# Kernel optimization log

Measured on AMD Instinct MI355X. Metric: run time of the kernel, lower is better.

## Reference

```python
import jax, jax.numpy as jnp
import numpy as np

V, N, D, K = 4, 2048, 128, 10
NEG = -1e9


def setup_inputs() -> dict:
    key = jax.random.key(0)
    k1, k2, k3, k4, k5 = jax.random.split(key, 5)
    aligned = jax.random.normal(k1, (V, N, D), dtype=jnp.float32)
    C = jax.random.uniform(k2, (V, V, N, N), dtype=jnp.float32)
    s = 1.0 / np.sqrt(D)
    WQ = jax.random.normal(k3, (V, D, D), dtype=jnp.float32) * s
    WK = jax.random.normal(k4, (V, D, D), dtype=jnp.float32) * s
    WV = jax.random.normal(k5, (V, D, D), dtype=jnp.float32) * s
    return {"aligned": aligned, "C": C, "WQ": WQ, "WK": WK, "WV": WV}


def _forward(aligned, C, WQ, WK, WV):
    # per-view linear projections (nn.Linear: x @ W^T), W: (V, out, in)
    Qn = jnp.einsum('vnd,ved->vne', aligned, WQ)  # (V,N,D)
    Kn = jnp.einsum('vnd,ved->vne', aligned, WK)
    Vn = jnp.einsum('vnd,ved->vne', aligned, WV)

    # per-pair row-wise top-k sparsify + row-normalize
    vals, idx = jax.lax.top_k(C, K)  # (V,V,N,K)
    pi = jnp.arange(V)[:, None, None, None]
    qi = jnp.arange(V)[None, :, None, None]
    ri = jnp.arange(N)[None, None, :, None]
    sparse = jnp.zeros_like(C).at[pi, qi, ri, idx].set(vals)
    row_sum = sparse.sum(axis=3, keepdims=True) + 1e-12
    C_hat = sparse / row_sum
    # diagonal (p == q) blocks stay all-zero in the original loop
    offdiag = (1.0 - jnp.eye(V, dtype=C.dtype))[:, :, None, None]
    C_hat = C_hat * offdiag

    # full pairwise scores (p queries attend to q keys)
    scores = jnp.einsum('pnd,qmd->pqnm', Qn, Kn) / jnp.sqrt(jnp.float32(D))
    mask = (C_hat > 0).astype(scores.dtype)
    scores = scores * mask + (1.0 - mask) * NEG
    alpha = jax.nn.softmax(scores, axis=3)  # (V,V,N,N)

    # aggregate: sum over source views q (diagonal gives uniform avg of Vn[p])
    nbr = jnp.einsum('pqnm,qmd->pnd', alpha, Vn)  # (V,N,D)
    return nbr


def reference(aligned, C, WQ, WK, WV):
    return _forward(aligned, C, WQ, WK, WV)
```

## Files before the change

### kernel.cpp

```cpp
#include <hip/hip_runtime.h>
#include <cstdint>
#include <cstddef>

#define VV 4
#define NN 2048
#define DDIM 128
#define KK 10
#define CAP 256

__device__ __forceinline__ bool kgt(float v1, int i1, float v0, int i0) {
  return (v1 > v0) || (v1 == v0 && i1 < i0);
}

__global__ __launch_bounds__(256) void proj_kernel(
    const float* __restrict__ A, const float* __restrict__ WQ,
    const float* __restrict__ WK, const float* __restrict__ WV,
    float* __restrict__ Qn, float* __restrict__ Kn, float* __restrict__ Vn,
    float* __restrict__ meanV)
{
  __shared__ float As[16][DDIM];
  __shared__ float Ws[3][16][129];
  __shared__ float s_mv[2][DDIM];

  const int t    = threadIdx.x;
  const int v    = blockIdx.x >> 7;
  const int n0   = (blockIdx.x & 127) * 16;
  const int e    = t & 127;
  const int half = t >> 7;

  float accq[8], acck[8], accv[8];
#pragma unroll
  for (int r = 0; r < 8; ++r) { accq[r] = 0.f; acck[r] = 0.f; accv[r] = 0.f; }

  const float* Ab = A + ((size_t)v * NN + n0) * DDIM;
#pragma unroll
  for (int k = 0; k < 2; ++k) {
    int id4 = k * 256 + t;
    int r   = id4 >> 5;
    int d4  = id4 & 31;
    float4 a4 = *(const float4*)(Ab + (size_t)id4 * 4);
    *(float4*)&As[r][d4 * 4] = a4;
  }
  const float* wqb = WQ + (size_t)v * DDIM * DDIM;
  const float* wkb = WK + (size_t)v * DDIM * DDIM;
  const float* wvb = WV + (size_t)v * DDIM * DDIM;

  for (int d0 = 0; d0 < DDIM; d0 += 16) {
    __syncthreads();
#pragma unroll
    for (int k = 0; k < 2; ++k) {
      int id4 = k * 256 + t;
      int ee  = id4 >> 2;
      int c4  = id4 & 3;
      const float4 wq4 = *(const float4*)(wqb + (size_t)ee * DDIM + d0 + c4 * 4);
      const float4 wk4 = *(const float4*)(wkb + (size_t)ee * DDIM + d0 + c4 * 4);
      const float4 wv4 = *(const float4*)(wvb + (size_t)ee * DDIM + d0 + c4 * 4);
      int dd = c4 * 4;
      Ws[0][dd + 0][ee] = wq4.x; Ws[0][dd + 1][ee] = wq4.y;
      Ws[0][dd + 2][ee] = wq4.z; Ws[0][dd + 3][ee] = wq4.w;
      Ws[1][dd + 0][ee] = wk4.x; Ws[1][dd + 1][ee] = wk4.y;
      Ws[1][dd + 2][ee] = wk4.z; Ws[1][dd + 3][ee] = wk4.w;
      Ws[2][dd + 0][ee] = wv4.x; Ws[2][dd + 1][ee] = wv4.y;
      Ws[2][dd + 2][ee] = wv4.z; Ws[2][dd + 3][ee] = wv4.w;
    }
    __syncthreads();
#pragma unroll
    for (int dd = 0; dd < 16; dd += 4) {
      float4 a[8];
#pragma unroll
      for (int r = 0; r < 8; ++r) a[r] = *(const float4*)&As[half * 8 + r][d0 + dd];
#pragma unroll
      for (int c = 0; c < 4; ++c) {
        float wq = Ws[0][dd + c][e];
        float wk = Ws[1][dd + c][e];
        float wv = Ws[2][dd + c][e];
#pragma unroll
        for (int r = 0; r < 8; ++r) {
          float av = ((const float*)&a[r])[c];
          accq[r] = fmaf(av, wq, accq[r]);
          acck[r] = fmaf(av, wk, acck[r]);
          accv[r] = fmaf(av, wv, accv[r]);
        }
      }
    }
  }

  const size_t ob = ((size_t)v * NN + n0 + half * 8) * DDIM + e;
#pragma unroll
  for (int r = 0; r < 8; ++r) {
    Qn[ob + (size_t)r * DDIM] = accq[r];
    Kn[ob + (size_t)r * DDIM] = acck[r];
    Vn[ob + (size_t)r * DDIM] = accv[r];
  }
  float s = 0.f;
#pragma unroll
  for (int r = 0; r < 8; ++r) s += accv[r];
  s_mv[half][e] = s;
  __syncthreads();
  if (half == 0)
    atomicAdd(&meanV[v * DDIM + e], (s + s_mv[1][e]) * (1.0f / 2048.0f));
}

__global__ __launch_bounds__(256) void topk_kernel(const float* __restrict__ C,
                                                   int* __restrict__ topIdx)
{
  __shared__ float    s_val[4][CAP];
  __shared__ int      s_idx[4][CAP];
  __shared__ unsigned s_cnt[4];

  const int t    = threadIdx.x;
  const int w    = t >> 6;
  const int lane = t & 63;
  const int task = blockIdx.x * 4 + w;
  const int pq   = task >> 11;
  const int n    = task & 2047;
  const int p    = (pq * 11) >> 5;
  const int o    = pq - p * 3;
  const int q    = o + (o >= p ? 1 : 0);

  const float* row = C + (((size_t)(p * 4 + q) * NN + n) << 11);
  float4 vv[8];
#pragma unroll
  for (int i = 0; i < 8; ++i) vv[i] = *(const float4*)(row + i * 256 + lane * 4);
  if (lane == 0) s_cnt[w] = 0u;

  const float T1 = 0.99f, T2 = 0.95f;
  int c1 = 0;
#pragma unroll
  for (int i = 0; i < 8; ++i) {
    const float* pv = (const float*)&vv[i];
#pragma unroll
    for (int c = 0; c < 4; ++c) c1 += (pv[c] > T1) ? 1 : 0;
  }
#pragma unroll
  for (int off = 32; off; off >>= 1) c1 += __shfl_xor(c1, off);

  float T = T1; int cnt = c1; bool ok = (c1 >= KK && c1 <= CAP);
  if (!ok) {
    int c2 = 0;
#pragma unroll
    for (int i = 0; i < 8; ++i) {
      const float* pv = (const float*)&vv[i];
#pragma unroll
      for (int c = 0; c < 4; ++c) c2 += (pv[c] > T2) ? 1 : 0;
    }
#pragma unroll
    for (int off = 32; off; off >>= 1) c2 += __shfl_xor(c2, off);
    T = T2; cnt = c2; ok = (c2 >= KK && c2 <= CAP);
  }

  int* outp = topIdx + (size_t)task * KK;

  if (ok) {
#pragma unroll
    for (int i = 0; i < 8; ++i) {
      const float* pv = (const float*)&vv[i];
#pragma unroll
      for (int c = 0; c < 4; ++c) {
        float x = pv[c];
        if (x > T) {
          unsigned pos = atomicAdd(&s_cnt[w], 1u);
          s_val[w][pos] = x;
          s_idx[w][pos] = i * 256 + lane * 4 + c;
        }
      }
    }
    __threadfence_block();
    if (cnt <= 64) {
      float kv = (lane < cnt) ? s_val[w][lane] : -1e30f;
      int   ki = (lane < cnt) ? s_idx[w][lane] : 0x7FFFFFFF;
#pragma unroll
      for (int k = 2; k <= 64; k <<= 1) {
#pragma unroll
        for (int j = k >> 1; j > 0; j >>= 1) {
          float ov = __shfl_xor(kv, j);
          int   oi = __shfl_xor(ki, j);
          bool dirDesc = (lane & k) == 0;
          bool lower   = (lane & j) == 0;
          bool ogt     = (ov > kv) || (ov == kv && oi < ki);
          bool take    = (dirDesc == lower) ? ogt : !ogt;
          if (take) { kv = ov; ki = oi; }
        }
      }
      if (lane < KK) outp[lane] = ki;
    } else {
      float rv[4]; int ri[4];
#pragma unroll
      for (int s = 0; s < 4; ++s) {
        int  sl = lane + s * 64;
        bool in = sl < cnt;
        rv[s] = in ? s_val[w][sl] : -1e30f;
        ri[s] = in ? s_idx[w][sl] : 0x7FFFFFFF;
      }
      for (int r = 0; r < KK; ++r) {
        float lv = rv[0]; int li = ri[0]; int ls = 0;
#pragma unroll
        for (int s = 1; s < 4; ++s)
          if (kgt(rv[s], ri[s], lv, li)) { lv = rv[s]; li = ri[s]; ls = s; }
        float mv = lv; int mi = li;
#pragma unroll
        for (int off = 1; off < 64; off <<= 1) {
          float ov = __shfl_xor(mv, off);
          int   oi = __shfl_xor(mi, off);
          if (kgt(ov, oi, mv, mi)) { mv = ov; mi = oi; }
        }
        if (lane == 0) outp[r] = mi;
        if (li == mi) {
#pragma unroll
          for (int s = 0; s < 4; ++s)
            if (ls == s) { rv[s] = -1e30f; ri[s] = 0x7FFFFFFF; }
        }
      }
    }
  } else {
    unsigned consumed = 0;
    for (int r = 0; r < KK; ++r) {
      float lv = -1e30f; int li = 0x7FFFFFFF; int ls = 0;
#pragma unroll
      for (int i = 0; i < 8; ++i) {
        const float* pv = (const float*)&vv[i];
#pragma unroll
        for (int c = 0; c < 4; ++c) {
          int   sl = i * 4 + c;
          float x  = ((consumed >> sl) & 1u) ? -1e30f : pv[c];
          int   ix = i * 256 + lane * 4 + c;
          if (kgt(x, ix, lv, li)) { lv = x; li = ix; ls = sl; }
        }
      }
      float mv = lv; int mi = li;
#pragma unroll
      for (int off = 1; off < 64; off <<= 1) {
        float ov = __shfl_xor(mv, off);
        int   oi = __shfl_xor(mi, off);
        if (kgt(ov, oi, mv, mi)) { mv = ov; mi = oi; }
      }
      if (lane == 0) outp[r] = mi;
      if (li == mi) consumed |= (1u << ls);
    }
  }
}

__global__ __launch_bounds__(256) void agg_kernel(
    const float* __restrict__ Qn, const float* __restrict__ Kn,
    const float* __restrict__ Vn, const float* __restrict__ meanV,
    const int* __restrict__ topIdx, float* __restrict__ out)
{
  __shared__ float s_sc[4][32];
  __shared__ float s_al[4][32];

  const int t    = threadIdx.x;
  const int w    = t >> 6;
  const int lane = t & 63;
  const int task = blockIdx.x * 4 + w;
  const int p    = task >> 11;
  const int n    = task & 2047;
  const float SCALE = 0.08838834764831845f;

  const float* qrow = Qn + ((size_t)p * NN + n) * DDIM;
  const float q0 = qrow[lane];
  const float q1 = qrow[lane + 64];

  int mAll[30];
#pragma unroll
  for (int o = 0; o < 3; ++o) {
    const int* ip = topIdx + ((size_t)(p * 3 + o) * NN + n) * KK;
#pragma unroll
    for (int j = 0; j < KK; ++j) mAll[o * KK + j] = ip[j];
  }

#pragma unroll
  for (int o = 0; o < 3; ++o) {
    const int q = o + (o >= p ? 1 : 0);
    const float* Kb = Kn + (size_t)q * NN * DDIM;
#pragma unroll
    for (int j = 0; j < KK; ++j) {
      const float* kr = Kb + (size_t)mAll[o * KK + j] * DDIM;
      float s = q0 * kr[lane] + q1 * kr[lane + 64];
#pragma unroll
      for (int off = 32; off; off >>= 1) s += __shfl_xor(s, off);
      if (lane == 0) s_sc[w][o * KK + j] = s * SCALE;
    }
  }
  __threadfence_block();

  if (lane < 30) {
    const int b = (lane / KK) * KK;
    float m = s_sc[w][b];
#pragma unroll
    for (int j = 1; j < KK; ++j) m = fmaxf(m, s_sc[w][b + j]);
    float den = 0.f;
#pragma unroll
    for (int j = 0; j < KK; ++j) den += expf(s_sc[w][b + j] - m);
    s_al[w][lane] = expf(s_sc[w][lane] - m) / den;
  }
  __threadfence_block();

  float acc0 = meanV[p * DDIM + lane];
  float acc1 = meanV[p * DDIM + lane + 64];
#pragma unroll
  for (int o = 0; o < 3; ++o) {
    const int q = o + (o >= p ? 1 : 0);
    const float* Vb = Vn + (size_t)q * NN * DDIM;
#pragma unroll
    for (int j = 0; j < KK; ++j) {
      const float a = s_al[w][o * KK + j];
      const float* vr = Vb + (size_t)mAll[o * KK + j] * DDIM;
      acc0 = fmaf(a, vr[lane], acc0);
      acc1 = fmaf(a, vr[lane + 64], acc1);
    }
  }
  float* orow = out + ((size_t)p * NN + n) * DDIM;
  orow[lane]      = acc0;
  orow[lane + 64] = acc1;
}

extern "C" void kernel_launch(void* const* d_in, const int* in_sizes, int n_in,
                              void* d_out, int out_size, void* d_ws, size_t ws_size,
                              hipStream_t stream)
{
  const float* A  = (const float*)d_in[0];
  const float* C  = (const float*)d_in[1];
  const float* WQ = (const float*)d_in[2];
  const float* WK = (const float*)d_in[3];
  const float* WV = (const float*)d_in[4];
  float* out = (float*)d_out;

  char* ws = (char*)d_ws;
  float* Qn    = (float*)ws;
  float* Kn    = (float*)(ws + (size_t)4 * 1024 * 1024);
  float* Vn    = (float*)(ws + (size_t)8 * 1024 * 1024);
  float* meanV = (float*)(ws + (size_t)12 * 1024 * 1024);
  int*   topIdx = (int*)(ws + (size_t)12 * 1024 * 1024 + 4096);

  hipMemsetAsync(meanV, 0, 512 * sizeof(float), stream);
  hipLaunchKernelGGL(proj_kernel, dim3(512), dim3(256), 0, stream,
                     A, WQ, WK, WV, Qn, Kn, Vn, meanV);
  hipLaunchKernelGGL(topk_kernel, dim3(6144), dim3(256), 0, stream, C, topIdx);
  hipLaunchKernelGGL(agg_kernel, dim3(2048), dim3(256), 0, stream,
                     Qn, Kn, Vn, meanV, topIdx, out);
}
```

Baseline: 415.5 us.

## Fuse top-k selection into aggregation kernel and replace mean atomics with partials

```diff
diff --git a/kernel.cpp b/kernel.cpp
--- a/kernel.cpp
+++ b/kernel.cpp
@@ -16,7 +16,7 @@
     const float* __restrict__ A, const float* __restrict__ WQ,
     const float* __restrict__ WK, const float* __restrict__ WV,
     float* __restrict__ Qn, float* __restrict__ Kn, float* __restrict__ Vn,
-    float* __restrict__ meanV)
+    float* __restrict__ partialMV)
 {
   __shared__ float As[16][DDIM];
   __shared__ float Ws[3][16][129];
@@ -24,7 +24,8 @@
 
   const int t    = threadIdx.x;
   const int v    = blockIdx.x >> 7;
-  const int n0   = (blockIdx.x & 127) * 16;
+  const int blk  = blockIdx.x & 127;
+  const int n0   = blk * 16;
   const int e    = t & 127;
   const int half = t >> 7;
 
@@ -98,155 +99,22 @@
   s_mv[half][e] = s;
   __syncthreads();
   if (half == 0)
-    atomicAdd(&meanV[v * DDIM + e], (s + s_mv[1][e]) * (1.0f / 2048.0f));
+    partialMV[((size_t)v * 128 + blk) * DDIM + e] = s + s_mv[1][e];
 }
 
-__global__ __launch_bounds__(256) void topk_kernel(const float* __restrict__ C,
-                                                   int* __restrict__ topIdx)
+__global__ __launch_bounds__(256) void fused_kernel(
+    const float* __restrict__ C, const float* __restrict__ Qn,
+    const float* __restrict__ Kn, const float* __restrict__ Vn,
+    const float* __restrict__ partialMV, float* __restrict__ out)
 {
   __shared__ float    s_val[4][CAP];
   __shared__ int      s_idx[4][CAP];
   __shared__ unsigned s_cnt[4];
-
-  const int t    = threadIdx.x;
-  const int w    = t >> 6;
-  const int lane = t & 63;
-  const int task = blockIdx.x * 4 + w;
-  const int pq   = task >> 11;
-  const int n    = task & 2047;
-  const int p    = (pq * 11) >> 5;
-  const int o    = pq - p * 3;
-  const int q    = o + (o >= p ? 1 : 0);
-
-  const float* row = C + (((size_t)(p * 4 + q) * NN + n) << 11);
-  float4 vv[8];
-#pragma unroll
-  for (int i = 0; i < 8; ++i) vv[i] = *(const float4*)(row + i * 256 + lane * 4);
-  if (lane == 0) s_cnt[w] = 0u;
-
-  const float T1 = 0.99f, T2 = 0.95f;
-  int c1 = 0;
-#pragma unroll
-  for (int i = 0; i < 8; ++i) {
-    const float* pv = (const float*)&vv[i];
-#pragma unroll
-    for (int c = 0; c < 4; ++c) c1 += (pv[c] > T1) ? 1 : 0;
-  }
-#pragma unroll
-  for (int off = 32; off; off >>= 1) c1 += __shfl_xor(c1, off);
-
-  float T = T1; int cnt = c1; bool ok = (c1 >= KK && c1 <= CAP);
-  if (!ok) {
-    int c2 = 0;
-#pragma unroll
-    for (int i = 0; i < 8; ++i) {
-      const float* pv = (const float*)&vv[i];
-#pragma unroll
-      for (int c = 0; c < 4; ++c) c2 += (pv[c] > T2) ? 1 : 0;
-    }
-#pragma unroll
-    for (int off = 32; off; off >>= 1) c2 += __shfl_xor(c2, off);
-    T = T2; cnt = c2; ok = (c2 >= KK && c2 <= CAP);
-  }
-
-  int* outp = topIdx + (size_t)task * KK;
-
-  if (ok) {
-#pragma unroll
-    for (int i = 0; i < 8; ++i) {
-      const float* pv = (const float*)&vv[i];
-#pragma unroll
-      for (int c = 0; c < 4; ++c) {
-        float x = pv[c];
-        if (x > T) {
-          unsigned pos = atomicAdd(&s_cnt[w], 1u);
-          s_val[w][pos] = x;
-          s_idx[w][pos] = i * 256 + lane * 4 + c;
-        }
-      }
-    }
-    __threadfence_block();
-    if (cnt <= 64) {
-      float kv = (lane < cnt) ? s_val[w][lane] : -1e30f;
-      int   ki = (lane < cnt) ? s_idx[w][lane] : 0x7FFFFFFF;
-#pragma unroll
-      for (int k = 2; k <= 64; k <<= 1) {
-#pragma unroll
-        for (int j = k >> 1; j > 0; j >>= 1) {
-          float ov = __shfl_xor(kv, j);
-          int   oi = __shfl_xor(ki, j);
-          bool dirDesc = (lane & k) == 0;
-          bool lower   = (lane & j) == 0;
-          bool ogt     = (ov > kv) || (ov == kv && oi < ki);
-          bool take    = (dirDesc == lower) ? ogt : !ogt;
-          if (take) { kv = ov; ki = oi; }
-        }
-      }
-      if (lane < KK) outp[lane] = ki;
-    } else {
-      float rv[4]; int ri[4];
-#pragma unroll
-      for (int s = 0; s < 4; ++s) {
-        int  sl = lane + s * 64;
-        bool in = sl < cnt;
-        rv[s] = in ? s_val[w][sl] : -1e30f;
-        ri[s] = in ? s_idx[w][sl] : 0x7FFFFFFF;
-      }
-      for (int r = 0; r < KK; ++r) {
-        float lv = rv[0]; int li = ri[0]; int ls = 0;
-#pragma unroll
-        for (int s = 1; s < 4; ++s)
-          if (kgt(rv[s], ri[s], lv, li)) { lv = rv[s]; li = ri[s]; ls = s; }
-        float mv = lv; int mi = li;
-#pragma unroll
-        for (int off = 1; off < 64; off <<= 1) {
-          float ov = __shfl_xor(mv, off);
-          int   oi = __shfl_xor(mi, off);
-          if (kgt(ov, oi, mv, mi)) { mv = ov; mi = oi; }
-        }
-        if (lane == 0) outp[r] = mi;
-        if (li == mi) {
-#pragma unroll
-          for (int s = 0; s < 4; ++s)
-            if (ls == s) { rv[s] = -1e30f; ri[s] = 0x7FFFFFFF; }
-        }
-      }
-    }
-  } else {
-    unsigned consumed = 0;
-    for (int r = 0; r < KK; ++r) {
-      float lv = -1e30f; int li = 0x7FFFFFFF; int ls = 0;
-#pragma unroll
-      for (int i = 0; i < 8; ++i) {
-        const float* pv = (const float*)&vv[i];
-#pragma unroll
-        for (int c = 0; c < 4; ++c) {
-          int   sl = i * 4 + c;
-          float x  = ((consumed >> sl) & 1u) ? -1e30f : pv[c];
-          int   ix = i * 256 + lane * 4 + c;
-          if (kgt(x, ix, lv, li)) { lv = x; li = ix; ls = sl; }
-        }
-      }
-      float mv = lv; int mi = li;
-#pragma unroll
-      for (int off = 1; off < 64; off <<= 1) {
-        float ov = __shfl_xor(mv, off);
-        int   oi = __shfl_xor(mi, off);
-        if (kgt(ov, oi, mv, mi)) { mv = ov; mi = oi; }
-      }
-      if (lane == 0) outp[r] = mi;
-      if (li == mi) consumed |= (1u << ls);
-    }
-  }
-}
-
-__global__ __launch_bounds__(256) void agg_kernel(
-    const float* __restrict__ Qn, const float* __restrict__ Kn,
-    const float* __restrict__ Vn, const float* __restrict__ meanV,
-    const int* __restrict__ topIdx, float* __restrict__ out)
-{
-  __shared__ float s_sc[4][32];
-  __shared__ float s_al[4][32];
+  __shared__ float    s_sc[4][32];
+  __shared__ float    s_al[4][32];
+  __shared__ int      s_sel[4][32];
+  __shared__ float    s_mvp[2][DDIM];
+  __shared__ float    s_mv[DDIM];
 
   const int t    = threadIdx.x;
   const int w    = t >> 6;
@@ -256,25 +124,153 @@
   const int n    = task & 2047;
   const float SCALE = 0.08838834764831845f;
 
+  {
+    const int e    = t & 127;
+    const int half = t >> 7;
+    const float* pb = partialMV + (size_t)p * 128 * DDIM;
+    float sum = 0.f;
+    for (int b = half * 64; b < half * 64 + 64; ++b)
+      sum += pb[(size_t)b * DDIM + e];
+    s_mvp[half][e] = sum;
+    __syncthreads();
+    if (half == 0) s_mv[e] = (s_mvp[0][e] + s_mvp[1][e]) * (1.0f / 2048.0f);
+    __syncthreads();
+  }
+
+  for (int o = 0; o < 3; ++o) {
+    const int q = o + (o >= p ? 1 : 0);
+    const float* row = C + (((size_t)(p * 4 + q) * NN + n) << 11);
+    float4 vv[8];
+#pragma unroll
+    for (int i = 0; i < 8; ++i) vv[i] = *(const float4*)(row + i * 256 + lane * 4);
+    if (lane == 0) s_cnt[w] = 0u;
+
+    const float T1 = 0.99f, T2 = 0.95f;
+    int c1 = 0;
+#pragma unroll
+    for (int i = 0; i < 8; ++i) {
+      const float* pv = (const float*)&vv[i];
+#pragma unroll
+      for (int c = 0; c < 4; ++c) c1 += (pv[c] > T1) ? 1 : 0;
+    }
+#pragma unroll
+    for (int off = 32; off; off >>= 1) c1 += __shfl_xor(c1, off);
+
+    float T = T1; int cnt = c1; bool ok = (c1 >= KK && c1 <= CAP);
+    if (!ok) {
+      int c2 = 0;
+#pragma unroll
+      for (int i = 0; i < 8; ++i) {
+        const float* pv = (const float*)&vv[i];
+#pragma unroll
+        for (int c = 0; c < 4; ++c) c2 += (pv[c] > T2) ? 1 : 0;
+      }
+#pragma unroll
+      for (int off = 32; off; off >>= 1) c2 += __shfl_xor(c2, off);
+      T = T2; cnt = c2; ok = (c2 >= KK && c2 <= CAP);
+    }
+
+    if (ok) {
+#pragma unroll
+      for (int i = 0; i < 8; ++i) {
+        const float* pv = (const float*)&vv[i];
+#pragma unroll
+        for (int c = 0; c < 4; ++c) {
+          float x = pv[c];
+          if (x > T) {
+            unsigned pos = atomicAdd(&s_cnt[w], 1u);
+            s_val[w][pos] = x;
+            s_idx[w][pos] = i * 256 + lane * 4 + c;
+          }
+        }
+      }
+      __threadfence_block();
+      if (cnt <= 64) {
+        float kv = (lane < cnt) ? s_val[w][lane] : -1e30f;
+        int   ki = (lane < cnt) ? s_idx[w][lane] : 0x7FFFFFFF;
+#pragma unroll
+        for (int k = 2; k <= 64; k <<= 1) {
+#pragma unroll
+          for (int j = k >> 1; j > 0; j >>= 1) {
+            float ov = __shfl_xor(kv, j);
+            int   oi = __shfl_xor(ki, j);
+            bool dirDesc = (lane & k) == 0;
+            bool lower   = (lane & j) == 0;
+            bool ogt     = (ov > kv) || (ov == kv && oi < ki);
+            bool take    = (dirDesc == lower) ? ogt : !ogt;
+            if (take) { kv = ov; ki = oi; }
+          }
+        }
+        if (lane < KK) s_sel[w][o * KK + lane] = ki;
+      } else {
+        float rv[4]; int ri[4];
+#pragma unroll
+        for (int s = 0; s < 4; ++s) {
+          int  sl = lane + s * 64;
+          bool in = sl < cnt;
+          rv[s] = in ? s_val[w][sl] : -1e30f;
+          ri[s] = in ? s_idx[w][sl] : 0x7FFFFFFF;
+        }
+        for (int r = 0; r < KK; ++r) {
+          float lv = rv[0]; int li = ri[0]; int ls = 0;
+#pragma unroll
+          for (int s = 1; s < 4; ++s)
+            if (kgt(rv[s], ri[s], lv, li)) { lv = rv[s]; li = ri[s]; ls = s; }
+          float mv = lv; int mi = li;
+#pragma unroll
+          for (int off = 1; off < 64; off <<= 1) {
+            float ov = __shfl_xor(mv, off);
+            int   oi = __shfl_xor(mi, off);
+            if (kgt(ov, oi, mv, mi)) { mv = ov; mi = oi; }
+          }
+          if (lane == 0) s_sel[w][o * KK + r] = mi;
+          if (li == mi) {
+#pragma unroll
+            for (int s = 0; s < 4; ++s)
+              if (ls == s) { rv[s] = -1e30f; ri[s] = 0x7FFFFFFF; }
+          }
+        }
+      }
+    } else {
+      unsigned consumed = 0;
+      for (int r = 0; r < KK; ++r) {
+        float lv = -1e30f; int li = 0x7FFFFFFF; int ls = 0;
+#pragma unroll
+        for (int i = 0; i < 8; ++i) {
+          const float* pv = (const float*)&vv[i];
+#pragma unroll
+          for (int c = 0; c < 4; ++c) {
+            int   sl = i * 4 + c;
+            float x  = ((consumed >> sl) & 1u) ? -1e30f : pv[c];
+            int   ix = i * 256 + lane * 4 + c;
+            if (kgt(x, ix, lv, li)) { lv = x; li = ix; ls = sl; }
+          }
+        }
+        float mv = lv; int mi = li;
+#pragma unroll
+        for (int off = 1; off < 64; off <<= 1) {
+          float ov = __shfl_xor(mv, off);
+          int   oi = __shfl_xor(mi, off);
+          if (kgt(ov, oi, mv, mi)) { mv = ov; mi = oi; }
+        }
+        if (lane == 0) s_sel[w][o * KK + r] = mi;
+        if (li == mi) consumed |= (1u << ls);
+      }
+    }
+    __threadfence_block();
+  }
+
   const float* qrow = Qn + ((size_t)p * NN + n) * DDIM;
   const float q0 = qrow[lane];
   const float q1 = qrow[lane + 64];
 
-  int mAll[30];
-#pragma unroll
-  for (int o = 0; o < 3; ++o) {
-    const int* ip = topIdx + ((size_t)(p * 3 + o) * NN + n) * KK;
-#pragma unroll
-    for (int j = 0; j < KK; ++j) mAll[o * KK + j] = ip[j];
-  }
-
 #pragma unroll
   for (int o = 0; o < 3; ++o) {
     const int q = o + (o >= p ? 1 : 0);
     const float* Kb = Kn + (size_t)q * NN * DDIM;
 #pragma unroll
     for (int j = 0; j < KK; ++j) {
-      const float* kr = Kb + (size_t)mAll[o * KK + j] * DDIM;
+      const float* kr = Kb + (size_t)s_sel[w][o * KK + j] * DDIM;
       float s = q0 * kr[lane] + q1 * kr[lane + 64];
 #pragma unroll
       for (int off = 32; off; off >>= 1) s += __shfl_xor(s, off);
@@ -295,8 +291,8 @@
   }
   __threadfence_block();
 
-  float acc0 = meanV[p * DDIM + lane];
-  float acc1 = meanV[p * DDIM + lane + 64];
+  float acc0 = s_mv[lane];
+  float acc1 = s_mv[lane + 64];
 #pragma unroll
   for (int o = 0; o < 3; ++o) {
     const int q = o + (o >= p ? 1 : 0);
@@ -304,7 +300,7 @@
 #pragma unroll
     for (int j = 0; j < KK; ++j) {
       const float a = s_al[w][o * KK + j];
-      const float* vr = Vb + (size_t)mAll[o * KK + j] * DDIM;
+      const float* vr = Vb + (size_t)s_sel[w][o * KK + j] * DDIM;
       acc0 = fmaf(a, vr[lane], acc0);
       acc1 = fmaf(a, vr[lane + 64], acc1);
     }
@@ -326,16 +322,13 @@
   float* out = (float*)d_out;
 
   char* ws = (char*)d_ws;
-  float* Qn    = (float*)ws;
-  float* Kn    = (float*)(ws + (size_t)4 * 1024 * 1024);
-  float* Vn    = (float*)(ws + (size_t)8 * 1024 * 1024);
-  float* meanV = (float*)(ws + (size_t)12 * 1024 * 1024);
-  int*   topIdx = (int*)(ws + (size_t)12 * 1024 * 1024 + 4096);
-
-  hipMemsetAsync(meanV, 0, 512 * sizeof(float), stream);
+  float* Qn        = (float*)ws;
+  float* Kn        = (float*)(ws + (size_t)4 * 1024 * 1024);
+  float* Vn        = (float*)(ws + (size_t)8 * 1024 * 1024);
+  float* partialMV = (float*)(ws + (size_t)12 * 1024 * 1024);
+
   hipLaunchKernelGGL(proj_kernel, dim3(512), dim3(256), 0, stream,
-                     A, WQ, WK, WV, Qn, Kn, Vn, meanV);
-  hipLaunchKernelGGL(topk_kernel, dim3(6144), dim3(256), 0, stream, C, topIdx);
-  hipLaunchKernelGGL(agg_kernel, dim3(2048), dim3(256), 0, stream,
-                     Qn, Kn, Vn, meanV, topIdx, out);
+                     A, WQ, WK, WV, Qn, Kn, Vn, partialMV);
+  hipLaunchKernelGGL(fused_kernel, dim3(2048), dim3(256), 0, stream,
+                     C, Qn, Kn, Vn, partialMV, out);
 }
```

Result: no change. 412.8 us (-0.6%).

## Fuse projection and top-k kernels into one launch, drop memset and atomics

Applied to the files above, without the earlier changes.

```diff
diff --git a/kernel.cpp b/kernel.cpp
--- a/kernel.cpp
+++ b/kernel.cpp
@@ -12,191 +12,210 @@
   return (v1 > v0) || (v1 == v0 && i1 < i0);
 }
 
-__global__ __launch_bounds__(256) void proj_kernel(
+struct ProjSm { float As[16][DDIM]; float s_mv[2][DDIM]; };
+struct TopkSm { float s_val[4][CAP]; int s_idx[4][CAP]; unsigned s_cnt[4]; };
+union SmU { ProjSm p; TopkSm t; };
+
+__global__ __launch_bounds__(256) void proj_topk_kernel(
     const float* __restrict__ A, const float* __restrict__ WQ,
     const float* __restrict__ WK, const float* __restrict__ WV,
+    const float* __restrict__ C,
     float* __restrict__ Qn, float* __restrict__ Kn, float* __restrict__ Vn,
-    float* __restrict__ meanV)
+    float* __restrict__ partialMV, int* __restrict__ topIdx)
 {
-  __shared__ float As[16][DDIM];
-  __shared__ float Ws[3][16][129];
-  __shared__ float s_mv[2][DDIM];
-
-  const int t    = threadIdx.x;
-  const int v    = blockIdx.x >> 7;
-  const int n0   = (blockIdx.x & 127) * 16;
-  const int e    = t & 127;
-  const int half = t >> 7;
-
-  float accq[8], acck[8], accv[8];
-#pragma unroll
-  for (int r = 0; r < 8; ++r) { accq[r] = 0.f; acck[r] = 0.f; accv[r] = 0.f; }
-
-  const float* Ab = A + ((size_t)v * NN + n0) * DDIM;
-#pragma unroll
-  for (int k = 0; k < 2; ++k) {
-    int id4 = k * 256 + t;
-    int r   = id4 >> 5;
-    int d4  = id4 & 31;
-    float4 a4 = *(const float4*)(Ab + (size_t)id4 * 4);
-    *(float4*)&As[r][d4 * 4] = a4;
-  }
-  const float* wqb = WQ + (size_t)v * DDIM * DDIM;
-  const float* wkb = WK + (size_t)v * DDIM * DDIM;
-  const float* wvb = WV + (size_t)v * DDIM * DDIM;
-
-  for (int d0 = 0; d0 < DDIM; d0 += 16) {
-    __syncthreads();
+  __shared__ SmU sm;
+  const int t = threadIdx.x;
+
+  if (blockIdx.x < 512) {
+    const int v    = blockIdx.x >> 7;
+    const int blk  = blockIdx.x & 127;
+    const int n0   = blk * 16;
+    const int e    = t & 127;
+    const int half = t >> 7;
+
+    const float* Ab = A + ((size_t)v * NN + n0) * DDIM;
 #pragma unroll
     for (int k = 0; k < 2; ++k) {
       int id4 = k * 256 + t;
-      int ee  = id4 >> 2;
-      int c4  = id4 & 3;
-      const float4 wq4 = *(const float4*)(wqb + (size_t)ee * DDIM + d0 + c4 * 4);
-      const float4 wk4 = *(const float4*)(wkb + (size_t)ee * DDIM + d0 + c4 * 4);
-      const float4 wv4 = *(const float4*)(wvb + (size_t)ee * DDIM + d0 + c4 * 4);
-      int dd = c4 * 4;
-      Ws[0][dd + 0][ee] = wq4.x; Ws[0][dd + 1][ee] = wq4.y;
-      Ws[0][dd + 2][ee] = wq4.z; Ws[0][dd + 3][ee] = wq4.w;
-      Ws[1][dd + 0][ee] = wk4.x; Ws[1][dd + 1][ee] = wk4.y;
-      Ws[1][dd + 2][ee] = wk4.z; Ws[1][dd + 3][ee] = wk4.w;
-      Ws[2][dd + 0][ee] = wv4.x; Ws[2][dd + 1][ee] = wv4.y;
-      Ws[2][dd + 2][ee] = wv4.z; Ws[2][dd + 3][ee] = wv4.w;
+      int r   = id4 >> 5;
+      int d4  = id4 & 31;
+      float4 a4 = *(const float4*)(Ab + (size_t)id4 * 4);
+      *(float4*)&sm.p.As[r][d4 * 4] = a4;
     }
     __syncthreads();
-#pragma unroll
-    for (int dd = 0; dd < 16; dd += 4) {
-      float4 a[8];
-#pragma unroll
-      for (int r = 0; r < 8; ++r) a[r] = *(const float4*)&As[half * 8 + r][d0 + dd];
-#pragma unroll
-      for (int c = 0; c < 4; ++c) {
-        float wq = Ws[0][dd + c][e];
-        float wk = Ws[1][dd + c][e];
-        float wv = Ws[2][dd + c][e];
-#pragma unroll
-        for (int r = 0; r < 8; ++r) {
-          float av = ((const float*)&a[r])[c];
-          accq[r] = fmaf(av, wq, accq[r]);
-          acck[r] = fmaf(av, wk, acck[r]);
-          accv[r] = fmaf(av, wv, accv[r]);
-        }
-      }
-    }
-  }
-
-  const size_t ob = ((size_t)v * NN + n0 + half * 8) * DDIM + e;
-#pragma unroll
-  for (int r = 0; r < 8; ++r) {
-    Qn[ob + (size_t)r * DDIM] = accq[r];
-    Kn[ob + (size_t)r * DDIM] = acck[r];
-    Vn[ob + (size_t)r * DDIM] = accv[r];
-  }
-  float s = 0.f;
-#pragma unroll
-  for (int r = 0; r < 8; ++r) s += accv[r];
-  s_mv[half][e] = s;
-  __syncthreads();
-  if (half == 0)
-    atomicAdd(&meanV[v * DDIM + e], (s + s_mv[1][e]) * (1.0f / 2048.0f));
-}
-
-__global__ __launch_bounds__(256) void topk_kernel(const float* __restrict__ C,
-                                                   int* __restrict__ topIdx)
-{
-  __shared__ float    s_val[4][CAP];
-  __shared__ int      s_idx[4][CAP];
-  __shared__ unsigned s_cnt[4];
-
-  const int t    = threadIdx.x;
-  const int w    = t >> 6;
-  const int lane = t & 63;
-  const int task = blockIdx.x * 4 + w;
-  const int pq   = task >> 11;
-  const int n    = task & 2047;
-  const int p    = (pq * 11) >> 5;
-  const int o    = pq - p * 3;
-  const int q    = o + (o >= p ? 1 : 0);
-
-  const float* row = C + (((size_t)(p * 4 + q) * NN + n) << 11);
-  float4 vv[8];
-#pragma unroll
-  for (int i = 0; i < 8; ++i) vv[i] = *(const float4*)(row + i * 256 + lane * 4);
-  if (lane == 0) s_cnt[w] = 0u;
-
-  const float T1 = 0.99f, T2 = 0.95f;
-  int c1 = 0;
-#pragma unroll
-  for (int i = 0; i < 8; ++i) {
-    const float* pv = (const float*)&vv[i];
-#pragma unroll
-    for (int c = 0; c < 4; ++c) c1 += (pv[c] > T1) ? 1 : 0;
-  }
-#pragma unroll
-  for (int off = 32; off; off >>= 1) c1 += __shfl_xor(c1, off);
-
-  float T = T1; int cnt = c1; bool ok = (c1 >= KK && c1 <= CAP);
-  if (!ok) {
-    int c2 = 0;
+
+    float accq[8], acck[8], accv[8];
+#pragma unroll
+    for (int r = 0; r < 8; ++r) { accq[r] = 0.f; acck[r] = 0.f; accv[r] = 0.f; }
+
+    const float* wqr = WQ + ((size_t)v * DDIM + e) * DDIM;
+    const float* wkr = WK + ((size_t)v * DDIM + e) * DDIM;
+    const float* wvr = WV + ((size_t)v * DDIM + e) * DDIM;
+
+    for (int d0 = 0; d0 < DDIM; d0 += 16) {
+      float4 wq4[4], wk4[4], wv4[4];
+#pragma unroll
+      for (int c4 = 0; c4 < 4; ++c4) {
+        wq4[c4] = *(const float4*)(wqr + d0 + c4 * 4);
+        wk4[c4] = *(const float4*)(wkr + d0 + c4 * 4);
+        wv4[c4] = *(const float4*)(wvr + d0 + c4 * 4);
+      }
+#pragma unroll
+      for (int g = 0; g < 4; ++g) {
+        float4 a4[8];
+#pragma unroll
+        for (int r = 0; r < 8; ++r)
+          a4[r] = *(const float4*)&sm.p.As[half * 8 + r][d0 + g * 4];
+#pragma unroll
+        for (int c = 0; c < 4; ++c) {
+          const float wq = ((const float*)&wq4[g])[c];
+          const float wk = ((const float*)&wk4[g])[c];
+          const float wv = ((const float*)&wv4[g])[c];
+#pragma unroll
+          for (int r = 0; r < 8; ++r) {
+            const float av = ((const float*)&a4[r])[c];
+            accq[r] = fmaf(av, wq, accq[r]);
+            acck[r] = fmaf(av, wk, acck[r]);
+            accv[r] = fmaf(av, wv, accv[r]);
+          }
+        }
+      }
+    }
+
+    const size_t ob = ((size_t)v * NN + n0 + half * 8) * DDIM + e;
+#pragma unroll
+    for (int r = 0; r < 8; ++r) {
+      Qn[ob + (size_t)r * DDIM] = accq[r];
+      Kn[ob + (size_t)r * DDIM] = acck[r];
+      Vn[ob + (size_t)r * DDIM] = accv[r];
+    }
+    float s = 0.f;
+#pragma unroll
+    for (int r = 0; r < 8; ++r) s += accv[r];
+    sm.p.s_mv[half][e] = s;
+    __syncthreads();
+    if (half == 0)
+      partialMV[((size_t)v * 128 + blk) * DDIM + e] = s + sm.p.s_mv[1][e];
+
+  } else {
+    const int w    = t >> 6;
+    const int lane = t & 63;
+    const int task = (blockIdx.x - 512) * 4 + w;
+    const int pq   = task >> 11;
+    const int n    = task & 2047;
+    const int p    = (pq * 11) >> 5;
+    const int o    = pq - p * 3;
+    const int q    = o + (o >= p ? 1 : 0);
+
+    const float* row = C + (((size_t)(p * 4 + q) * NN + n) << 11);
+    float4 vv[8];
+#pragma unroll
+    for (int i = 0; i < 8; ++i) vv[i] = *(const float4*)(row + i * 256 + lane * 4);
+    if (lane == 0) sm.t.s_cnt[w] = 0u;
+
+    const float T1 = 0.99f, T2 = 0.95f;
+    int c1 = 0;
 #pragma unroll
     for (int i = 0; i < 8; ++i) {
       const float* pv = (const float*)&vv[i];
 #pragma unroll
-      for (int c = 0; c < 4; ++c) c2 += (pv[c] > T2) ? 1 : 0;
-    }
-#pragma unroll
-    for (int off = 32; off; off >>= 1) c2 += __shfl_xor(c2, off);
-    T = T2; cnt = c2; ok = (c2 >= KK && c2 <= CAP);
-  }
-
-  int* outp = topIdx + (size_t)task * KK;
-
-  if (ok) {
-#pragma unroll
-    for (int i = 0; i < 8; ++i) {
-      const float* pv = (const float*)&vv[i];
-#pragma unroll
-      for (int c = 0; c < 4; ++c) {
-        float x = pv[c];
-        if (x > T) {
-          unsigned pos = atomicAdd(&s_cnt[w], 1u);
-          s_val[w][pos] = x;
-          s_idx[w][pos] = i * 256 + lane * 4 + c;
-        }
-      }
-    }
-    __threadfence_block();
-    if (cnt <= 64) {
-      float kv = (lane < cnt) ? s_val[w][lane] : -1e30f;
-      int   ki = (lane < cnt) ? s_idx[w][lane] : 0x7FFFFFFF;
-#pragma unroll
-      for (int k = 2; k <= 64; k <<= 1) {
-#pragma unroll
-        for (int j = k >> 1; j > 0; j >>= 1) {
-          float ov = __shfl_xor(kv, j);
-          int   oi = __shfl_xor(ki, j);
-          bool dirDesc = (lane & k) == 0;
-          bool lower   = (lane & j) == 0;
-          bool ogt     = (ov > kv) || (ov == kv && oi < ki);
-          bool take    = (dirDesc == lower) ? ogt : !ogt;
-          if (take) { kv = ov; ki = oi; }
-        }
-      }
-      if (lane < KK) outp[lane] = ki;
+      for (int c = 0; c < 4; ++c) c1 += (pv[c] > T1) ? 1 : 0;
+    }
+#pragma unroll
+    for (int off = 32; off; off >>= 1) c1 += __shfl_xor(c1, off);
+
+    float T = T1; int cnt = c1; bool ok = (c1 >= KK && c1 <= CAP);
+    if (!ok) {
+      int c2 = 0;
+#pragma unroll
+      for (int i = 0; i < 8; ++i) {
+        const float* pv = (const float*)&vv[i];
+#pragma unroll
+        for (int c = 0; c < 4; ++c) c2 += (pv[c] > T2) ? 1 : 0;
+      }
+#pragma unroll
+      for (int off = 32; off; off >>= 1) c2 += __shfl_xor(c2, off);
+      T = T2; cnt = c2; ok = (c2 >= KK && c2 <= CAP);
+    }
+
+    int* outp = topIdx + (size_t)task * KK;
+
+    if (ok) {
+#pragma unroll
+      for (int i = 0; i < 8; ++i) {
+        const float* pv = (const float*)&vv[i];
+#pragma unroll
+        for (int c = 0; c < 4; ++c) {
+          float x = pv[c];
+          if (x > T) {
+            unsigned pos = atomicAdd(&sm.t.s_cnt[w], 1u);
+            sm.t.s_val[w][pos] = x;
+            sm.t.s_idx[w][pos] = i * 256 + lane * 4 + c;
+          }
+        }
+      }
+      __threadfence_block();
+      if (cnt <= 64) {
+        float kv = (lane < cnt) ? sm.t.s_val[w][lane] : -1e30f;
+        int   ki = (lane < cnt) ? sm.t.s_idx[w][lane] : 0x7FFFFFFF;
+#pragma unroll
+        for (int k = 2; k <= 64; k <<= 1) {
+#pragma unroll
+          for (int j = k >> 1; j > 0; j >>= 1) {
+            float ov = __shfl_xor(kv, j);
+            int   oi = __shfl_xor(ki, j);
+            bool dirDesc = (lane & k) == 0;
+            bool lower   = (lane & j) == 0;
+            bool ogt     = (ov > kv) || (ov == kv && oi < ki);
+            bool take    = (dirDesc == lower) ? ogt : !ogt;
+            if (take) { kv = ov; ki = oi; }
+          }
+        }
+        if (lane < KK) outp[lane] = ki;
+      } else {
+        float rv[4]; int ri[4];
+#pragma unroll
+        for (int s = 0; s < 4; ++s) {
+          int  sl = lane + s * 64;
+          bool in = sl < cnt;
+          rv[s] = in ? sm.t.s_val[w][sl] : -1e30f;
+          ri[s] = in ? sm.t.s_idx[w][sl] : 0x7FFFFFFF;
+        }
+        for (int r = 0; r < KK; ++r) {
+          float lv = rv[0]; int li = ri[0]; int ls = 0;
+#pragma unroll
+          for (int s = 1; s < 4; ++s)
+            if (kgt(rv[s], ri[s], lv, li)) { lv = rv[s]; li = ri[s]; ls = s; }
+          float mv = lv; int mi = li;
+#pragma unroll
+          for (int off = 1; off < 64; off <<= 1) {
+            float ov = __shfl_xor(mv, off);
+            int   oi = __shfl_xor(mi, off);
+            if (kgt(ov, oi, mv, mi)) { mv = ov; mi = oi; }
+          }
+          if (lane == 0) outp[r] = mi;
+          if (li == mi) {
+#pragma unroll
+            for (int s = 0; s < 4; ++s)
+              if (ls == s) { rv[s] = -1e30f; ri[s] = 0x7FFFFFFF; }
+          }
+        }
+      }
     } else {
-      float rv[4]; int ri[4];
-#pragma unroll
-      for (int s = 0; s < 4; ++s) {
-        int  sl = lane + s * 64;
-        bool in = sl < cnt;
-        rv[s] = in ? s_val[w][sl] : -1e30f;
-        ri[s] = in ? s_idx[w][sl] : 0x7FFFFFFF;
-      }
+      unsigned consumed = 0;
       for (int r = 0; r < KK; ++r) {
-        float lv = rv[0]; int li = ri[0]; int ls = 0;
-#pragma unroll
-        for (int s = 1; s < 4; ++s)
-          if (kgt(rv[s], ri[s], lv, li)) { lv = rv[s]; li = ri[s]; ls = s; }
+        float lv = -1e30f; int li = 0x7FFFFFFF; int ls = 0;
+#pragma unroll
+        for (int i = 0; i < 8; ++i) {
+          const float* pv = (const float*)&vv[i];
+#pragma unroll
+          for (int c = 0; c < 4; ++c) {
+            int   sl = i * 4 + c;
+            float x  = ((consumed >> sl) & 1u) ? -1e30f : pv[c];
+            int   ix = i * 256 + lane * 4 + c;
+            if (kgt(x, ix, lv, li)) { lv = x; li = ix; ls = sl; }
+          }
+        }
         float mv = lv; int mi = li;
 #pragma unroll
         for (int off = 1; off < 64; off <<= 1) {
@@ -205,48 +224,21 @@
           if (kgt(ov, oi, mv, mi)) { mv = ov; mi = oi; }
         }
         if (lane == 0) outp[r] = mi;
-        if (li == mi) {
-#pragma unroll
-          for (int s = 0; s < 4; ++s)
-            if (ls == s) { rv[s] = -1e30f; ri[s] = 0x7FFFFFFF; }
-        }
-      }
-    }
-  } else {
-    unsigned consumed = 0;
-    for (int r = 0; r < KK; ++r) {
-      float lv = -1e30f; int li = 0x7FFFFFFF; int ls = 0;
-#pragma unroll
-      for (int i = 0; i < 8; ++i) {
-        const float* pv = (const float*)&vv[i];
-#pragma unroll
-        for (int c = 0; c < 4; ++c) {
-          int   sl = i * 4 + c;
-          float x  = ((consumed >> sl) & 1u) ? -1e30f : pv[c];
-          int   ix = i * 256 + lane * 4 + c;
-          if (kgt(x, ix, lv, li)) { lv = x; li = ix; ls = sl; }
-        }
-      }
-      float mv = lv; int mi = li;
-#pragma unroll
-      for (int off = 1; off < 64; off <<= 1) {
-        float ov = __shfl_xor(mv, off);
-        int   oi = __shfl_xor(mi, off);
-        if (kgt(ov, oi, mv, mi)) { mv = ov; mi = oi; }
-      }
-      if (lane == 0) outp[r] = mi;
-      if (li == mi) consumed |= (1u << ls);
+        if (li == mi) consumed |= (1u << ls);
+      }
     }
   }
 }
 
 __global__ __launch_bounds__(256) void agg_kernel(
     const float* __restrict__ Qn, const float* __restrict__ Kn,
-    const float* __restrict__ Vn, const float* __restrict__ meanV,
+    const float* __restrict__ Vn, const float* __restrict__ partialMV,
     const int* __restrict__ topIdx, float* __restrict__ out)
 {
   __shared__ float s_sc[4][32];
   __shared__ float s_al[4][32];
+  __shared__ float s_mvp[2][DDIM];
+  __shared__ float s_mv[DDIM];
 
   const int t    = threadIdx.x;
   const int w    = t >> 6;
@@ -256,6 +248,19 @@
   const int n    = task & 2047;
   const float SCALE = 0.08838834764831845f;
 
+  {
+    const int e    = t & 127;
+    const int half = t >> 7;
+    const float* pb = partialMV + (size_t)p * 128 * DDIM;
+    float sum = 0.f;
+    for (int b = half * 64; b < half * 64 + 64; ++b)
+      sum += pb[(size_t)b * DDIM + e];
+    s_mvp[half][e] = sum;
+    __syncthreads();
+    if (half == 0) s_mv[e] = (s_mvp[0][e] + s_mvp[1][e]) * (1.0f / 2048.0f);
+    __syncthreads();
+  }
+
   const float* qrow = Qn + ((size_t)p * NN + n) * DDIM;
   const float q0 = qrow[lane];
   const float q1 = qrow[lane + 64];
@@ -263,7 +268,7 @@
   int mAll[30];
 #pragma unroll
   for (int o = 0; o < 3; ++o) {
-    const int* ip = topIdx + ((size_t)(p * 3 + o) * NN + n) * KK;
+    const int* ip = topIdx + ((size_t)((p * 3 + o) * NN + n)) * KK;
 #pragma unroll
     for (int j = 0; j < KK; ++j) mAll[o * KK + j] = ip[j];
   }
@@ -295,8 +300,8 @@
   }
   __threadfence_block();
 
-  float acc0 = meanV[p * DDIM + lane];
-  float acc1 = meanV[p * DDIM + lane + 64];
+  float acc0 = s_mv[lane];
+  float acc1 = s_mv[lane + 64];
 #pragma unroll
   for (int o = 0; o < 3; ++o) {
     const int q = o + (o >= p ? 1 : 0);
@@ -326,16 +331,14 @@
   float* out = (float*)d_out;
 
   char* ws = (char*)d_ws;
-  float* Qn    = (float*)ws;
-  float* Kn    = (float*)(ws + (size_t)4 * 1024 * 1024);
-  float* Vn    = (float*)(ws + (size_t)8 * 1024 * 1024);
-  float* meanV = (float*)(ws + (size_t)12 * 1024 * 1024);
-  int*   topIdx = (int*)(ws + (size_t)12 * 1024 * 1024 + 4096);
-
-  hipMemsetAsync(meanV, 0, 512 * sizeof(float), stream);
-  hipLaunchKernelGGL(proj_kernel, dim3(512), dim3(256), 0, stream,
-                     A, WQ, WK, WV, Qn, Kn, Vn, meanV);
-  hipLaunchKernelGGL(topk_kernel, dim3(6144), dim3(256), 0, stream, C, topIdx);
+  float* Qn        = (float*)ws;
+  float* Kn        = (float*)(ws + (size_t)4 * 1024 * 1024);
+  float* Vn        = (float*)(ws + (size_t)8 * 1024 * 1024);
+  float* partialMV = (float*)(ws + (size_t)12 * 1024 * 1024);
+  int*   topIdx    = (int*)(ws + (size_t)12 * 1024 * 1024 + 256 * 1024);
+
+  hipLaunchKernelGGL(proj_topk_kernel, dim3(6656), dim3(256), 0, stream,
+                     A, WQ, WK, WV, C, Qn, Kn, Vn, partialMV, topIdx);
   hipLaunchKernelGGL(agg_kernel, dim3(2048), dim3(256), 0, stream,
-                     Qn, Kn, Vn, meanV, topIdx, out);
+                     Qn, Kn, Vn, partialMV, topIdx, out);
 }
```

Result: no change. 414.2 us (-0.3%).
